# Performance work log

Hardware: AMD Instinct MI355X
Metric: run time of the kernel (lower is better)

Reference implementation:

```python
import jax, jax.numpy as jnp
import numpy as np

B, NX, NC, D, H = 2, 512, 4096, 1024, 16
HD = D // H  # head_dim = context_dim // heads
LN_EPS = 1e-5


def setup_inputs() -> dict:
    key = jax.random.key(0)
    k0, k1, k2, k3, k4 = jax.random.split(key, 5)
    x = jax.random.normal(k0, (B, NX, D), dtype=jnp.float32)
    c = jax.random.normal(k1, (B, NC, D), dtype=jnp.float32)
    attn_mask = jax.random.randint(k2, (B, NX, NC), 0, 2).astype(bool)
    # learned params
    ln_w = jnp.ones((D,), jnp.float32)
    ln_b = jnp.zeros((D,), jnp.float32)
    Wq = jax.random.normal(k3, (D, D), dtype=jnp.float32) * 0.02  # to_q (query_dim -> inner_dim)
    Wo = jax.random.normal(k4, (D, D), dtype=jnp.float32) * 0.02  # to_out (inner_dim -> query_dim)
    return {"x": x, "c": c, "attn_mask": attn_mask, "ln_w": ln_w, "ln_b": ln_b, "Wq": Wq, "Wo": Wo}


def _layernorm(x, w, b):
    mu = jnp.mean(x, axis=-1, keepdims=True)
    var = jnp.mean(jnp.square(x - mu), axis=-1, keepdims=True)
    return (x - mu) * jax.lax.rsqrt(var + LN_EPS) * w + b


def reference(x, c, attn_mask, ln_w, ln_b, Wq, Wo):
    scale = HD ** (-0.5)
    xn = _layernorm(x, ln_w, ln_b)
    q = (xn @ Wq).reshape(B, NX, H, HD).transpose(0, 2, 1, 3)      # (B,H,NX,HD)
    kv0 = c.reshape(B, NC, H, HD).transpose(0, 2, 1, 3)             # (B,H,NC,HD) -- kvt=(kv0,kv0)
    kv = jnp.concatenate([q, kv0], axis=2)                          # kv_append_q=True -> (B,H,NX+NC,HD)
    # mask: ones for the appended-q block, user mask for context block
    m = jnp.broadcast_to(attn_mask[:, None, :, :], (B, H, NX, NC))
    full_mask = jnp.concatenate([jnp.ones((B, H, NX, NX), bool), m], axis=-1)
    sim = jnp.einsum('bhqd,bhkd->bhqk', q * scale, kv)              # (B,H,NX,NX+NC)
    neg = -jnp.finfo(sim.dtype).max
    sim = jnp.where(full_mask, sim, neg)
    attn = jax.nn.softmax(sim, axis=-1)
    a = jnp.einsum('bhqk,bhkd->bhqd', attn, kv)
    o = a.transpose(0, 2, 1, 3).reshape(B, NX, H * HD) @ Wo
    return (o, kv0)
```

## Files before the change

### kernel.cpp

```cpp
#include <hip/hip_runtime.h>

#define B_  2
#define NX_ 512
#define NC_ 4096
#define D_  1024
#define H_  16
#define HD_ 64
#define NT_ (NX_ + NC_)
#define NSPLIT 4
#define KBS (NT_ / 64 / NSPLIT)

typedef float  floatx4  __attribute__((ext_vector_type(4)));
typedef __bf16 bf16x8   __attribute__((ext_vector_type(8)));
typedef unsigned short ushort8v __attribute__((ext_vector_type(8)));

__device__ __forceinline__ bf16x8 as_bf16x8(ushort8v u) {
    union { ushort8v u; bf16x8 b; } c; c.u = u; return c.b;
}
__device__ __forceinline__ unsigned short f2bf(float f) {
    unsigned u = __float_as_uint(f);
    u += 0x7FFF + ((u >> 16) & 1);
    return (unsigned short)(u >> 16);
}

__global__ __launch_bounds__(256)
void prep_kernel(const float* __restrict__ x, const float* __restrict__ lw,
                 const float* __restrict__ lb, const float* __restrict__ Wq,
                 const float* __restrict__ Wo, const int* __restrict__ mask,
                 const float* __restrict__ c,
                 unsigned short* __restrict__ xnb, unsigned short* __restrict__ WqT,
                 unsigned short* __restrict__ WoT, unsigned* __restrict__ bits,
                 unsigned short* __restrict__ cbf, float* __restrict__ gz) {
    int blk = blockIdx.x;
    int tid = threadIdx.x;
    if (blk < 1024) {
        int row = blk;
        float4 v = reinterpret_cast<const float4*>(x)[(size_t)row * (D_ / 4) + tid];
        float s  = v.x + v.y + v.z + v.w;
        float s2 = v.x * v.x + v.y * v.y + v.z * v.z + v.w * v.w;
        #pragma unroll
        for (int off = 32; off > 0; off >>= 1) {
            s  += __shfl_down(s, off);
            s2 += __shfl_down(s2, off);
        }
        __shared__ float sm[4], sm2[4], stat[2];
        int wv = tid >> 6;
        if ((tid & 63) == 0) { sm[wv] = s; sm2[wv] = s2; }
        __syncthreads();
        if (tid == 0) {
            float S  = sm[0] + sm[1] + sm[2] + sm[3];
            float S2 = sm2[0] + sm2[1] + sm2[2] + sm2[3];
            float mu  = S * (1.0f / D_);
            float var = fmaxf(S2 * (1.0f / D_) - mu * mu, 0.0f);
            stat[0] = mu;
            stat[1] = rsqrtf(var + 1e-5f);
        }
        __syncthreads();
        float mu = stat[0], rs = stat[1];
        float4 w4 = reinterpret_cast<const float4*>(lw)[tid];
        float4 b4 = reinterpret_cast<const float4*>(lb)[tid];
        ushort4 o;
        o.x = f2bf((v.x - mu) * rs * w4.x + b4.x);
        o.y = f2bf((v.y - mu) * rs * w4.y + b4.y);
        o.z = f2bf((v.z - mu) * rs * w4.z + b4.z);
        o.w = f2bf((v.w - mu) * rs * w4.w + b4.w);
        reinterpret_cast<ushort4*>(xnb)[(size_t)row * (D_ / 4) + tid] = o;
    } else if (blk < 1536) {
        int which = (blk - 1024) >> 8;
        int t = (blk - 1024) & 255;
        const float* W = which ? Wo : Wq;
        unsigned short* WT = which ? WoT : WqT;
        __shared__ unsigned short T[64][72];
        int row0 = (t >> 4) * 64, col0 = (t & 15) * 64;
        int r = tid >> 2, ch = (tid & 3) * 16;
        const float* src = W + (size_t)(row0 + r) * D_ + col0 + ch;
        unsigned short vals[16];
        #pragma unroll
        for (int k = 0; k < 4; ++k) {
            float4 v = reinterpret_cast<const float4*>(src)[k];
            vals[k*4+0] = f2bf(v.x); vals[k*4+1] = f2bf(v.y);
            vals[k*4+2] = f2bf(v.z); vals[k*4+3] = f2bf(v.w);
        }
        #pragma unroll
        for (int i = 0; i < 16; ++i) T[ch + i][r] = vals[i];
        __syncthreads();
        unsigned short* dst = WT + (size_t)(col0 + r) * D_ + row0 + ch;
        uint4 o0 = *reinterpret_cast<uint4*>(&T[r][ch]);
        uint4 o1 = *reinterpret_cast<uint4*>(&T[r][ch + 8]);
        *reinterpret_cast<uint4*>(dst)     = o0;
        *reinterpret_cast<uint4*>(dst + 8) = o1;
    } else if (blk < 2048) {
        size_t w = (size_t)(blk - 1536) * 256 + tid;
        const int* src = mask + w * 32;
        unsigned b = 0;
        #pragma unroll
        for (int k = 0; k < 8; ++k) {
            int4 v = reinterpret_cast<const int4*>(src)[k];
            b |= (v.x != 0 ? 1u : 0u) << (k * 4 + 0);
            b |= (v.y != 0 ? 1u : 0u) << (k * 4 + 1);
            b |= (v.z != 0 ? 1u : 0u) << (k * 4 + 2);
            b |= (v.w != 0 ? 1u : 0u) << (k * 4 + 3);
        }
        bits[w] = b;
    } else if (blk < 10240) {
        size_t i = ((size_t)(blk - 2048) * 256 + tid) * 4;
        float4 v = *reinterpret_cast<const float4*>(c + i);
        ushort4 o;
        o.x = f2bf(v.x); o.y = f2bf(v.y); o.z = f2bf(v.z); o.w = f2bf(v.w);
        *reinterpret_cast<ushort4*>(cbf + i) = o;
    } else {
        size_t i = ((size_t)(blk - 10240) * 256 + tid) * 4;
        float4 z = {0.f, 0.f, 0.f, 0.f};
        *reinterpret_cast<float4*>(gz + i) = z;
    }
}

__global__ __launch_bounds__(256)
void kv0_kernel(const float* __restrict__ c, float* __restrict__ out2) {
    size_t i = (size_t)blockIdx.x * 256 + threadIdx.x;
    int d4 = (int)(i & 15);
    size_t r = i >> 4;
    int n = (int)(r % NC_);
    size_t r2 = r / NC_;
    int h = (int)(r2 & (H_ - 1));
    int b = (int)(r2 >> 4);
    float4 v = *reinterpret_cast<const float4*>(c + ((size_t)(b * NC_ + n)) * D_ + h * HD_ + d4 * 4);
    reinterpret_cast<float4*>(out2)[i] = v;
}

__global__ __launch_bounds__(256)
void gemm_bt_kernel(const unsigned short* __restrict__ A, const unsigned short* __restrict__ BT,
                    unsigned short* __restrict__ Cb) {
    __shared__ unsigned short As[64][72];
    __shared__ unsigned short Bs[64][72];
    int tid = threadIdx.x;
    int lane = tid & 63, wave = tid >> 6;
    int m16 = lane & 15, g = lane >> 4, g8 = g * 8;
    int row0 = blockIdx.y * 64, col0 = blockIdx.x * 64;
    int r = tid >> 2, ch = (tid & 3) * 16;

    floatx4 acc[4];
    #pragma unroll
    for (int t = 0; t < 4; ++t) acc[t] = (floatx4){0.f, 0.f, 0.f, 0.f};

    for (int kc = 0; kc < 16; ++kc) {
        int k0 = kc * 64;
        const unsigned short* asrc = A  + (size_t)(row0 + r) * D_ + k0 + ch;
        const unsigned short* bsrc = BT + (size_t)(col0 + r) * D_ + k0 + ch;
        uint4 a0 = *reinterpret_cast<const uint4*>(asrc);
        uint4 a1 = *reinterpret_cast<const uint4*>(asrc + 8);
        uint4 b0 = *reinterpret_cast<const uint4*>(bsrc);
        uint4 b1 = *reinterpret_cast<const uint4*>(bsrc + 8);
        *reinterpret_cast<uint4*>(&As[r][ch])     = a0;
        *reinterpret_cast<uint4*>(&As[r][ch + 8]) = a1;
        *reinterpret_cast<uint4*>(&Bs[r][ch])     = b0;
        *reinterpret_cast<uint4*>(&Bs[r][ch + 8]) = b1;
        __syncthreads();
        bf16x8 fa0 = as_bf16x8(*reinterpret_cast<ushort8v*>(&As[16 * wave + m16][g8]));
        bf16x8 fa1 = as_bf16x8(*reinterpret_cast<ushort8v*>(&As[16 * wave + m16][32 + g8]));
        #pragma unroll
        for (int t = 0; t < 4; ++t) {
            bf16x8 fb0 = as_bf16x8(*reinterpret_cast<ushort8v*>(&Bs[16 * t + m16][g8]));
            bf16x8 fb1 = as_bf16x8(*reinterpret_cast<ushort8v*>(&Bs[16 * t + m16][32 + g8]));
            acc[t] = __builtin_amdgcn_mfma_f32_16x16x32_bf16(fa0, fb0, acc[t], 0, 0, 0);
            acc[t] = __builtin_amdgcn_mfma_f32_16x16x32_bf16(fa1, fb1, acc[t], 0, 0, 0);
        }
        __syncthreads();
    }
    #pragma unroll
    for (int t = 0; t < 4; ++t)
        #pragma unroll
        for (int reg = 0; reg < 4; ++reg)
            Cb[(size_t)(row0 + 16 * wave + g * 4 + reg) * D_ + col0 + 16 * t + m16] = f2bf(acc[t][reg]);
}

__global__ __launch_bounds__(256)
void gemm_attn_kernel(const float* __restrict__ gacc, const float* __restrict__ gacc_l,
                      const unsigned short* __restrict__ BT, float* __restrict__ out) {
    __shared__ unsigned short As[64][72];
    __shared__ unsigned short Bs[64][72];
    int tid = threadIdx.x;
    int lane = tid & 63, wave = tid >> 6;
    int m16 = lane & 15, g = lane >> 4, g8 = g * 8;
    int row0 = blockIdx.y * 64, col0 = blockIdx.x * 64;
    int r = tid >> 2, ch = (tid & 3) * 16;

    floatx4 acc[4];
    #pragma unroll
    for (int t = 0; t < 4; ++t) acc[t] = (floatx4){0.f, 0.f, 0.f, 0.f};

    for (int kc = 0; kc < 16; ++kc) {
        int k0 = kc * 64;
        int row = row0 + r;
        float inv = 1.0f / fmaxf(gacc_l[(size_t)row * H_ + kc], 1e-35f);
        const float* asrc = gacc + (size_t)row * D_ + k0 + ch;
        const unsigned short* bsrc = BT + (size_t)(col0 + r) * D_ + k0 + ch;
        unsigned short av[16];
        #pragma unroll
        for (int t = 0; t < 4; ++t) {
            float4 v = reinterpret_cast<const float4*>(asrc)[t];
            av[t*4+0] = f2bf(v.x * inv); av[t*4+1] = f2bf(v.y * inv);
            av[t*4+2] = f2bf(v.z * inv); av[t*4+3] = f2bf(v.w * inv);
        }
        uint4 b0 = *reinterpret_cast<const uint4*>(bsrc);
        uint4 b1 = *reinterpret_cast<const uint4*>(bsrc + 8);
        *reinterpret_cast<uint4*>(&As[r][ch])     = *reinterpret_cast<uint4*>(&av[0]);
        *reinterpret_cast<uint4*>(&As[r][ch + 8]) = *reinterpret_cast<uint4*>(&av[8]);
        *reinterpret_cast<uint4*>(&Bs[r][ch])     = b0;
        *reinterpret_cast<uint4*>(&Bs[r][ch + 8]) = b1;
        __syncthreads();
        bf16x8 fa0 = as_bf16x8(*reinterpret_cast<ushort8v*>(&As[16 * wave + m16][g8]));
        bf16x8 fa1 = as_bf16x8(*reinterpret_cast<ushort8v*>(&As[16 * wave + m16][32 + g8]));
        #pragma unroll
        for (int t = 0; t < 4; ++t) {
            bf16x8 fb0 = as_bf16x8(*reinterpret_cast<ushort8v*>(&Bs[16 * t + m16][g8]));
            bf16x8 fb1 = as_bf16x8(*reinterpret_cast<ushort8v*>(&Bs[16 * t + m16][32 + g8]));
            acc[t] = __builtin_amdgcn_mfma_f32_16x16x32_bf16(fa0, fb0, acc[t], 0, 0, 0);
            acc[t] = __builtin_amdgcn_mfma_f32_16x16x32_bf16(fa1, fb1, acc[t], 0, 0, 0);
        }
        __syncthreads();
    }
    #pragma unroll
    for (int t = 0; t < 4; ++t)
        #pragma unroll
        for (int reg = 0; reg < 4; ++reg)
            out[(size_t)(row0 + 16 * wave + g * 4 + reg) * D_ + col0 + 16 * t + m16] = acc[t][reg];
}

__global__ __launch_bounds__(256, 4)
void attn_kernel(const unsigned short* __restrict__ qbf,
                 const unsigned short* __restrict__ cbf,
                 const unsigned* __restrict__ maskbits,
                 float* __restrict__ gacc, float* __restrict__ gacc_l) {
    int blk   = blockIdx.x;
    int bh    = ((blk >> 8) << 3) | (blk & 7);
    int inner = (blk >> 3) & 31;
    int qt    = inner & 7;
    int split = inner >> 3;
    int h  = bh & 15;
    int b  = bh >> 4;
    int tid  = threadIdx.x;
    int lane = tid & 63;
    int wave = tid >> 6;
    int m16  = lane & 15;
    int g    = lane >> 4;
    int g8   = g * 8;

    __shared__ unsigned short Ks [64][72];
    __shared__ unsigned short Kts[64][72];
    __shared__ unsigned short Ps [64][64];

    const unsigned short* qrow = qbf + ((size_t)(b * NX_ + qt * 64 + 16 * wave + m16)) * D_ + h * HD_;
    bf16x8 qa0 = as_bf16x8(*reinterpret_cast<const ushort8v*>(qrow + g8));
    bf16x8 qa1 = as_bf16x8(*reinterpret_cast<const ushort8v*>(qrow + 32 + g8));

    floatx4 acc_o[4];
    #pragma unroll
    for (int td = 0; td < 4; ++td) acc_o[td] = (floatx4){0.f, 0.f, 0.f, 0.f};
    floatx4 acc_l = (floatx4){0.f, 0.f, 0.f, 0.f};

    ushort8v ones_u;
    #pragma unroll
    for (int j = 0; j < 8; ++j) ones_u[j] = 0x3F80;
    bf16x8 onesf = as_bf16x8(ones_u);

    int Kg = tid >> 4;
    int Dg = tid & 15;
    int pcst = ((Kg >> 1) + (Dg >> 1)) & 7;
    int prsw = 2 * ((m16 >> 2) & 3);

    for (int i = 0; i < KBS; ++i) {
        int kb = split * KBS + i;
        __syncthreads();
        const unsigned short* src = (kb < 8)
            ? qbf + ((size_t)(b * NX_ + kb * 64 + 4 * Kg)) * D_ + h * HD_ + 4 * Dg
            : cbf + ((size_t)(b * NC_ + kb * 64 - NX_ + 4 * Kg)) * D_ + h * HD_ + 4 * Dg;
        uint2 rows[4];
        #pragma unroll
        for (int kk = 0; kk < 4; ++kk)
            rows[kk] = *reinterpret_cast<const uint2*>(src + (size_t)kk * D_);
        #pragma unroll
        for (int kk = 0; kk < 4; ++kk)
            *reinterpret_cast<uint2*>(&Ks[4 * Kg + kk][4 * Dg]) = rows[kk];
        #pragma unroll
        for (int i2 = 0; i2 < 4; ++i2) {
            unsigned sel = (i2 & 1) ? 0x07060302u : 0x05040100u;
            unsigned r0 = (i2 >> 1) ? rows[0].y : rows[0].x;
            unsigned r1 = (i2 >> 1) ? rows[1].y : rows[1].x;
            unsigned r2 = (i2 >> 1) ? rows[2].y : rows[2].x;
            unsigned r3 = (i2 >> 1) ? rows[3].y : rows[3].x;
            uint2 cw;
            cw.x = __builtin_amdgcn_perm(r1, r0, sel);
            cw.y = __builtin_amdgcn_perm(r3, r2, sel);
            *reinterpret_cast<uint2*>(&Kts[4 * Dg + i2][pcst * 8 + 4 * (Kg & 1)]) = cw;
        }
        __syncthreads();

        floatx4 accs[4];
        #pragma unroll
        for (int t = 0; t < 4; ++t) {
            bf16x8 b0 = as_bf16x8(*reinterpret_cast<ushort8v*>(&Ks[16 * t + m16][g8]));
            bf16x8 b1 = as_bf16x8(*reinterpret_cast<ushort8v*>(&Ks[16 * t + m16][32 + g8]));
            floatx4 d = (floatx4){0.f, 0.f, 0.f, 0.f};
            d = __builtin_amdgcn_mfma_f32_16x16x32_bf16(qa0, b0, d, 0, 0, 0);
            d = __builtin_amdgcn_mfma_f32_16x16x32_bf16(qa1, b1, d, 0, 0, 0);
            accs[t] = d;
        }

        unsigned mw0[4], mw1[4];
        if (kb >= 8) {
            #pragma unroll
            for (int r = 0; r < 4; ++r) {
                size_t mi = ((size_t)(b * NX_ + qt * 64 + 16 * wave + g * 4 + r)) * (NC_ / 32)
                          + (size_t)(kb - 8) * 2;
                uint2 w = *reinterpret_cast<const uint2*>(&maskbits[mi]);
                mw0[r] = w.x; mw1[r] = w.y;
            }
        }

        const float C1 = 0.18033688011112042f;
        const float C2 = 92.33248261689366f;
        #pragma unroll
        for (int t = 0; t < 4; ++t) {
            int cc = 2 * t + (m16 >> 3);
            #pragma unroll
            for (int r = 0; r < 4; ++r) {
                float e = fminf(accs[t][r] * C1, C2) - C2;
                float p = __builtin_amdgcn_exp2f(e);
                if (kb >= 8) {
                    unsigned w = (t < 2) ? mw0[r] : mw1[r];
                    unsigned bit = (w >> ((16 * t + m16) & 31)) & 1u;
                    p = bit ? p : 0.0f;
                }
                int prow = 16 * wave + g * 4 + r;
                int pc = (cc + 2 * g) & 7;
                Ps[prow][pc * 8 + (m16 & 7)] = (unsigned short)(__float_as_uint(p) >> 16);
            }
        }
        asm volatile("s_waitcnt lgkmcnt(0)" ::: "memory");

        bf16x8 p0 = as_bf16x8(*reinterpret_cast<ushort8v*>(&Ps[16 * wave + m16][((g + prsw) & 7) * 8]));
        bf16x8 p1 = as_bf16x8(*reinterpret_cast<ushort8v*>(&Ps[16 * wave + m16][((4 + g + prsw) & 7) * 8]));
        acc_l = __builtin_amdgcn_mfma_f32_16x16x32_bf16(p0, onesf, acc_l, 0, 0, 0);
        acc_l = __builtin_amdgcn_mfma_f32_16x16x32_bf16(p1, onesf, acc_l, 0, 0, 0);
        #pragma unroll
        for (int td = 0; td < 4; ++td) {
            int row = 16 * td + m16;
            int rh = row >> 3;
            bf16x8 v0 = as_bf16x8(*reinterpret_cast<ushort8v*>(&Kts[row][((g + rh) & 7) * 8]));
            bf16x8 v1 = as_bf16x8(*reinterpret_cast<ushort8v*>(&Kts[row][((4 + g + rh) & 7) * 8]));
            acc_o[td] = __builtin_amdgcn_mfma_f32_16x16x32_bf16(p0, v0, acc_o[td], 0, 0, 0);
            acc_o[td] = __builtin_amdgcn_mfma_f32_16x16x32_bf16(p1, v1, acc_o[td], 0, 0, 0);
        }
    }

    #pragma unroll
    for (int r = 0; r < 4; ++r) {
        int qrow_ = qt * 64 + 16 * wave + g * 4 + r;
        float* dst = gacc + ((size_t)(b * NX_ + qrow_)) * D_ + h * HD_;
        #pragma unroll
        for (int td = 0; td < 4; ++td)
            unsafeAtomicAdd(&dst[16 * td + m16], acc_o[td][r]);
        if (m16 == 0)
            unsafeAtomicAdd(&gacc_l[(size_t)(b * NX_ + qrow_) * H_ + h], acc_l[r]);
    }
}

extern "C" void kernel_launch(void* const* d_in, const int* in_sizes, int n_in,
                              void* d_out, int out_size, void* d_ws, size_t ws_size,
                              hipStream_t stream) {
    (void)in_sizes; (void)n_in; (void)out_size; (void)d_ws; (void)ws_size;
    const float* x    = (const float*)d_in[0];
    const float* c    = (const float*)d_in[1];
    const int*   mask = (const int*)d_in[2];
    const float* ln_w = (const float*)d_in[3];
    const float* ln_b = (const float*)d_in[4];
    const float* Wq   = (const float*)d_in[5];
    const float* Wo   = (const float*)d_in[6];
    float* out  = (float*)d_out;
    float* out2 = out + (size_t)B_ * NX_ * D_;

    float* base = out2;
    unsigned short* qbf      = (unsigned short*)(base);
    unsigned*       maskbits = (unsigned*)(base + 524288);
    float*          gacc     = base + 655360;
    float*          gacc_l   = base + 1703936;
    unsigned short* WqT      = (unsigned short*)(base + 1720320);
    unsigned short* WoT      = (unsigned short*)(base + 2244608);
    unsigned short* xnb      = (unsigned short*)(base + 2768896);
    unsigned short* cbf      = (unsigned short*)(base + 3817472);

    prep_kernel<<<11280, 256, 0, stream>>>(x, ln_w, ln_b, Wq, Wo, mask, c,
                                           xnb, WqT, WoT, maskbits, cbf, gacc);
    gemm_bt_kernel<<<dim3(16, 16), 256, 0, stream>>>(xnb, WqT, qbf);
    attn_kernel<<<NSPLIT * 256, 256, 0, stream>>>(qbf, cbf, maskbits, gacc, gacc_l);
    gemm_attn_kernel<<<dim3(16, 16), 256, 0, stream>>>(gacc, gacc_l, WoT, out);
    kv0_kernel<<<(B_ * H_ * NC_ * HD_ / 4) / 256, 256, 0, stream>>>(c, out2);
}
```

Measured before the change: 207.6 us.

## Prefetch next K tile, raise split count, fuse kv0 copy into prep

Raises the attention key-split from 4 to 6 and the occupancy hint to 6 blocks per CU, remapping block indices so XCD grouping still holds. K/V rows for the next tile are register-prefetched while the current tile is staged in LDS, and mask loads move before the barrier. When a workspace is available, scratch buffers move there and the kv0 transpose copy is fused into the c-to-bf16 conversion in prep, dropping a separate kernel launch. The exp argument is computed with a single fma and clamp. The extra splits add more atomic traffic, and the higher occupancy target may cause register spills.

```diff
diff --git a/kernel.cpp b/kernel.cpp
--- a/kernel.cpp
+++ b/kernel.cpp
@@ -7,7 +7,7 @@
 #define H_  16
 #define HD_ 64
 #define NT_ (NX_ + NC_)
-#define NSPLIT 4
+#define NSPLIT 6
 #define KBS (NT_ / 64 / NSPLIT)
 
 typedef float  floatx4  __attribute__((ext_vector_type(4)));
@@ -30,7 +30,8 @@
                  const float* __restrict__ c,
                  unsigned short* __restrict__ xnb, unsigned short* __restrict__ WqT,
                  unsigned short* __restrict__ WoT, unsigned* __restrict__ bits,
-                 unsigned short* __restrict__ cbf, float* __restrict__ gz) {
+                 unsigned short* __restrict__ cbf, float* __restrict__ gz,
+                 float* __restrict__ kv0o) {
     int blk = blockIdx.x;
     int tid = threadIdx.x;
     if (blk < 1024) {
@@ -108,6 +109,15 @@
         ushort4 o;
         o.x = f2bf(v.x); o.y = f2bf(v.y); o.z = f2bf(v.z); o.w = f2bf(v.w);
         *reinterpret_cast<ushort4*>(cbf + i) = o;
+        if (kv0o != nullptr) {
+            size_t row = i >> 10;
+            int dd = (int)(i & 1023);
+            int hh = dd >> 6, d4 = (dd & 63) >> 2;
+            int bb = (int)(row >> 12);
+            int n  = (int)(row & 4095);
+            size_t o4 = (((size_t)(bb * 16 + hh) * NC_ + n) << 4) + d4;
+            reinterpret_cast<float4*>(kv0o)[o4] = v;
+        }
     } else {
         size_t i = ((size_t)(blk - 10240) * 256 + tid) * 4;
         float4 z = {0.f, 0.f, 0.f, 0.f};
@@ -227,14 +237,17 @@
             out[(size_t)(row0 + 16 * wave + g * 4 + reg) * D_ + col0 + 16 * t + m16] = acc[t][reg];
 }
 
-__global__ __launch_bounds__(256, 4)
+__global__ __launch_bounds__(256, 6)
 void attn_kernel(const unsigned short* __restrict__ qbf,
                  const unsigned short* __restrict__ cbf,
                  const unsigned* __restrict__ maskbits,
                  float* __restrict__ gacc, float* __restrict__ gacc_l) {
     int blk   = blockIdx.x;
-    int bh    = ((blk >> 8) << 3) | (blk & 7);
-    int inner = (blk >> 3) & 31;
+    int xcd   = blk & 7;
+    int rest  = blk >> 3;
+    int grp   = rest / 48;
+    int inner = rest - grp * 48;
+    int bh    = grp * 8 + xcd;
     int qt    = inner & 7;
     int split = inner >> 3;
     int h  = bh & 15;
@@ -269,16 +282,33 @@
     int pcst = ((Kg >> 1) + (Dg >> 1)) & 7;
     int prsw = 2 * ((m16 >> 2) & 3);
 
+    int kb0 = split * KBS;
+
+    uint2 rows[4];
+    {
+        const unsigned short* s0 = (kb0 < 8)
+            ? qbf + ((size_t)(b * NX_ + kb0 * 64 + 4 * Kg)) * D_ + h * HD_ + 4 * Dg
+            : cbf + ((size_t)(b * NC_ + kb0 * 64 - NX_ + 4 * Kg)) * D_ + h * HD_ + 4 * Dg;
+        #pragma unroll
+        for (int kk = 0; kk < 4; ++kk)
+            rows[kk] = *reinterpret_cast<const uint2*>(s0 + (size_t)kk * D_);
+    }
+
     for (int i = 0; i < KBS; ++i) {
-        int kb = split * KBS + i;
-        __syncthreads();
-        const unsigned short* src = (kb < 8)
-            ? qbf + ((size_t)(b * NX_ + kb * 64 + 4 * Kg)) * D_ + h * HD_ + 4 * Dg
-            : cbf + ((size_t)(b * NC_ + kb * 64 - NX_ + 4 * Kg)) * D_ + h * HD_ + 4 * Dg;
-        uint2 rows[4];
-        #pragma unroll
-        for (int kk = 0; kk < 4; ++kk)
-            rows[kk] = *reinterpret_cast<const uint2*>(src + (size_t)kk * D_);
+        int kb = kb0 + i;
+        __syncthreads();
+
+        unsigned mw0[4], mw1[4];
+        if (kb >= 8) {
+            #pragma unroll
+            for (int r = 0; r < 4; ++r) {
+                size_t mi = ((size_t)(b * NX_ + qt * 64 + 16 * wave + g * 4 + r)) * (NC_ / 32)
+                          + (size_t)(kb - 8) * 2;
+                uint2 w = *reinterpret_cast<const uint2*>(&maskbits[mi]);
+                mw0[r] = w.x; mw1[r] = w.y;
+            }
+        }
+
         #pragma unroll
         for (int kk = 0; kk < 4; ++kk)
             *reinterpret_cast<uint2*>(&Ks[4 * Kg + kk][4 * Dg]) = rows[kk];
@@ -294,7 +324,21 @@
             cw.y = __builtin_amdgcn_perm(r3, r2, sel);
             *reinterpret_cast<uint2*>(&Kts[4 * Dg + i2][pcst * 8 + 4 * (Kg & 1)]) = cw;
         }
-        __syncthreads();
+
+        {
+            int kbn = (i + 1 < KBS) ? kb + 1 : kb;
+            const unsigned short* sn = (kbn < 8)
+                ? qbf + ((size_t)(b * NX_ + kbn * 64 + 4 * Kg)) * D_ + h * HD_ + 4 * Dg
+                : cbf + ((size_t)(b * NC_ + kbn * 64 - NX_ + 4 * Kg)) * D_ + h * HD_ + 4 * Dg;
+            #pragma unroll
+            for (int kk = 0; kk < 4; ++kk)
+                rows[kk] = *reinterpret_cast<const uint2*>(sn + (size_t)kk * D_);
+        }
+
+        asm volatile("s_waitcnt lgkmcnt(0)" ::: "memory");
+        __builtin_amdgcn_s_barrier();
+        __builtin_amdgcn_sched_barrier(0);
+        asm volatile("" ::: "memory");
 
         floatx4 accs[4];
         #pragma unroll
@@ -307,17 +351,6 @@
             accs[t] = d;
         }
 
-        unsigned mw0[4], mw1[4];
-        if (kb >= 8) {
-            #pragma unroll
-            for (int r = 0; r < 4; ++r) {
-                size_t mi = ((size_t)(b * NX_ + qt * 64 + 16 * wave + g * 4 + r)) * (NC_ / 32)
-                          + (size_t)(kb - 8) * 2;
-                uint2 w = *reinterpret_cast<const uint2*>(&maskbits[mi]);
-                mw0[r] = w.x; mw1[r] = w.y;
-            }
-        }
-
         const float C1 = 0.18033688011112042f;
         const float C2 = 92.33248261689366f;
         #pragma unroll
@@ -325,7 +358,7 @@
             int cc = 2 * t + (m16 >> 3);
             #pragma unroll
             for (int r = 0; r < 4; ++r) {
-                float e = fminf(accs[t][r] * C1, C2) - C2;
+                float e = fminf(fmaf(accs[t][r], C1, -C2), 0.0f);
                 float p = __builtin_amdgcn_exp2f(e);
                 if (kb >= 8) {
                     unsigned w = (t < 2) ? mw0[r] : mw1[r];
@@ -369,7 +402,7 @@
 extern "C" void kernel_launch(void* const* d_in, const int* in_sizes, int n_in,
                               void* d_out, int out_size, void* d_ws, size_t ws_size,
                               hipStream_t stream) {
-    (void)in_sizes; (void)n_in; (void)out_size; (void)d_ws; (void)ws_size;
+    (void)in_sizes; (void)n_in; (void)out_size;
     const float* x    = (const float*)d_in[0];
     const float* c    = (const float*)d_in[1];
     const int*   mask = (const int*)d_in[2];
@@ -380,7 +413,10 @@
     float* out  = (float*)d_out;
     float* out2 = out + (size_t)B_ * NX_ * D_;
 
-    float* base = out2;
+    const size_t SCRATCH_FLOATS = 8011776;
+    bool use_ws = (d_ws != nullptr) && (ws_size >= SCRATCH_FLOATS * sizeof(float));
+    float* base = use_ws ? (float*)d_ws : out2;
+
     unsigned short* qbf      = (unsigned short*)(base);
     unsigned*       maskbits = (unsigned*)(base + 524288);
     float*          gacc     = base + 655360;
@@ -391,9 +427,11 @@
     unsigned short* cbf      = (unsigned short*)(base + 3817472);
 
     prep_kernel<<<11280, 256, 0, stream>>>(x, ln_w, ln_b, Wq, Wo, mask, c,
-                                           xnb, WqT, WoT, maskbits, cbf, gacc);
+                                           xnb, WqT, WoT, maskbits, cbf, gacc,
+                                           use_ws ? out2 : nullptr);
     gemm_bt_kernel<<<dim3(16, 16), 256, 0, stream>>>(xnb, WqT, qbf);
     attn_kernel<<<NSPLIT * 256, 256, 0, stream>>>(qbf, cbf, maskbits, gacc, gacc_l);
     gemm_attn_kernel<<<dim3(16, 16), 256, 0, stream>>>(gacc, gacc_l, WoT, out);
-    kv0_kernel<<<(B_ * H_ * NC_ * HD_ / 4) / 256, 256, 0, stream>>>(c, out2);
-}
+    if (!use_ws)
+        kv0_kernel<<<(B_ * H_ * NC_ * HD_ / 4) / 256, 256, 0, stream>>>(c, out2);
+}
```

New measurement: 223.3 us. +7.6%, slower.
